# Kernel optimization log

Measured on AMD Instinct MI355X. Metric: run time of the kernel, lower is better.

The kernel has to match this reference:

```python
import jax, jax.numpy as jnp
import numpy as np

NEG_SLOPE = 0.01  # nn.LeakyReLU default

def leaky(x):
    return jnp.where(x >= 0, x, NEG_SLOPE * x)

def setup_inputs() -> dict:
    key = jax.random.key(0)
    ks = jax.random.split(key, 10)
    N, E, IN_DIM, OUT_DIM = 100000, 1600000, 128, 128
    indices = jax.random.randint(ks[0], (2, E), 0, N, dtype=jnp.int64 if jax.config.jax_enable_x64 else jnp.int32)
    features = jax.random.normal(ks[1], (N, IN_DIM), dtype=jnp.float32)
    s = 1.0 / np.sqrt(IN_DIM)
    W_att_w = jax.random.uniform(ks[2], (OUT_DIM, IN_DIM), minval=-s, maxval=s)
    W_att_b = jax.random.uniform(ks[3], (OUT_DIM,), minval=-s, maxval=s)
    W1_w = jax.random.uniform(ks[4], (OUT_DIM, IN_DIM), minval=-s, maxval=s)
    W1_b = jax.random.uniform(ks[5], (OUT_DIM,), minval=-s, maxval=s)
    W2_w = jax.random.uniform(ks[6], (OUT_DIM, OUT_DIM), minval=-s, maxval=s)
    W2_b = jax.random.uniform(ks[7], (OUT_DIM,), minval=-s, maxval=s)
    # xavier_uniform for a: gain*sqrt(6/(fan_in+fan_out)), fan_in=2*OUT_DIM, fan_out=1
    lim = float(np.sqrt(6.0 / (2 * OUT_DIM + 1)))
    a = jax.random.uniform(ks[8], (2 * OUT_DIM, 1), minval=-lim, maxval=lim)
    return {"indices": indices, "features": features, "num_nodes": N,
            "W_att_w": W_att_w, "W_att_b": W_att_b, "W1_w": W1_w, "W1_b": W1_b,
            "W2_w": W2_w, "W2_b": W2_b, "a": a}

def reference(indices, features, num_nodes, W_att_w, W_att_b, W1_w, W1_b, W2_w, W2_b, a):
    src, dst = indices[0], indices[1]
    out_dim = W_att_w.shape[0]
    # h_trans = W_att(features)
    h_trans = features @ W_att_w.T + W_att_b  # [N, D]
    # cat([src_h, dst_h]) @ a  ==  src_h @ a[:D] + dst_h @ a[D:]  (avoids materializing cat)
    a_src, a_dst = a[:out_dim], a[out_dim:]
    logits = leaky(h_trans[src] @ a_src + h_trans[dst] @ a_dst)  # [E, 1]
    # edge softmax over incoming edges of each dst (raw exp, as in original)
    exp_l = jnp.exp(logits)
    denom = jax.ops.segment_sum(exp_l, dst, num_segments=num_nodes)  # [N, 1]
    alpha = exp_l / (denom[dst] + 1e-9)  # [E, 1]
    # sparse.mm(adj_att, W1(features)) == segment_sum of alpha * msg[src] over dst
    h_msg = features @ W1_w.T + W1_b  # [N, D]
    h_neigh = jax.ops.segment_sum(alpha * h_msg[src], dst, num_segments=num_nodes)  # [N, D]
    h_self = features  # in_dim == out_dim branch
    term1 = h_self + h_neigh
    term2 = (h_self * h_neigh) @ W2_w.T + W2_b
    return leaky(term1 + term2)
```

## Files before the change

### kernel.cpp

```cpp
#include <hip/hip_runtime.h>

#define D 128
#define CAP 2560
typedef __attribute__((ext_vector_type(8))) short short8;
typedef __attribute__((ext_vector_type(4))) float f32x4;

__device__ __forceinline__ float leaky(float x){ return x >= 0.f ? x : 0.01f*x; }
__device__ __forceinline__ unsigned short f2bf(float x){
    unsigned u = __float_as_uint(x);
    u = (u + 0x7fffu + ((u>>16)&1u)) >> 16;
    return (unsigned short)u;
}
__device__ __forceinline__ short8 pack8m(f32x4 a, f32x4 b){
    short8 s;
    s[0]=(short)f2bf(a[0]); s[1]=(short)f2bf(a[1]);
    s[2]=(short)f2bf(a[2]); s[3]=(short)f2bf(a[3]);
    s[4]=(short)f2bf(b[0]); s[5]=(short)f2bf(b[1]);
    s[6]=(short)f2bf(b[2]); s[7]=(short)f2bf(b[3]);
    return s;
}

__global__ void k_prep(const float* __restrict__ Ww, const float* __restrict__ Wb,
                       const float* __restrict__ a, float* __restrict__ v,
                       const float* __restrict__ W1, const float* __restrict__ W2,
                       unsigned short* __restrict__ W1b, unsigned short* __restrict__ W2b){
    int b = blockIdx.x;
    if(b < 64){
        int i = b*256 + threadIdx.x;
        W1b[i] = f2bf(W1[i]);
        W2b[i] = f2bf(W2[i]);
        return;
    }
    int i = threadIdx.x; if(i >= 128) return;
    float vs=0.f, vd=0.f;
    for (int o=0;o<D;++o){ float w = Ww[o*D+i]; vs = fmaf(w, a[o], vs); vd = fmaf(w, a[D+o], vd); }
    v[i]=vs; v[D+i]=vd;
    if(i==0){
        float cs=0.f,cd=0.f;
        for(int o=0;o<D;++o){ cs=fmaf(Wb[o],a[o],cs); cd=fmaf(Wb[o],a[D+o],cd); }
        v[256]=cs; v[257]=cd;
    }
}

__global__ __launch_bounds__(256) void k_msgscal(const float* __restrict__ F,
        const unsigned short* __restrict__ W1b, const float* __restrict__ b1,
        const float* __restrict__ v, unsigned short* __restrict__ Hp,
        float* __restrict__ ss, float* __restrict__ sd, int N,
        const int* __restrict__ dst, unsigned* __restrict__ M,
        int E, int GT, int CHUNK, int NB){
    __shared__ __align__(16) unsigned short Wlds[17408];
    if((int)blockIdx.x >= GT){
        unsigned* h = (unsigned*)Wlds;
        for(int i=threadIdx.x;i<NB;i+=256) h[i]=0u;
        __syncthreads();
        int blk = (int)blockIdx.x - GT;
        int s = blk*CHUNK;
        int e = s+CHUNK < E ? s+CHUNK : E;
        for(int i=s+(int)threadIdx.x;i<e;i+=256) atomicAdd(&h[((unsigned)dst[i])>>6],1u);
        __syncthreads();
        for(int j=threadIdx.x;j<NB;j+=256) M[(size_t)j*256 + blk] = h[j];
        return;
    }
    #pragma unroll
    for(int k=0;k<8;++k){
        int idx = ((int)threadIdx.x + k*256)*8;
        int row = idx >> 7, col = idx & 127;
        *(short8*)(&Wlds[row*136 + col]) = *(const short8*)(W1b + idx);
    }
    __syncthreads();
    const int lane = threadIdx.x & 63, wv = threadIdx.x>>6;
    const int t = lane & 15, g = lane >> 4;
    float bb[8];
    #pragma unroll
    for(int j=0;j<8;++j) bb[j] = b1[j*16+t];
    const float c_s = v[256], c_d = v[257];
    const int Mt = (N+15)>>4;
    for(int rt = (int)blockIdx.x*4 + wv; rt < Mt; rt += GT*4){
        int row0 = rt*16 + t;
        int row = row0 < N ? row0 : N-1;
        const float* fr = F + (size_t)row*D + g*8;
        f32x4 acc[8];
        #pragma unroll
        for(int j=0;j<8;++j) acc[j] = (f32x4){0.f,0.f,0.f,0.f};
        float ds = 0.f, dd = 0.f;
        #pragma unroll
        for(int kk=0;kk<4;++kk){
            f32x4 lo = *(const f32x4*)(fr + kk*32);
            f32x4 hi = *(const f32x4*)(fr + kk*32 + 4);
            f32x4 vsl = *(const f32x4*)(v + kk*32 + g*8);
            f32x4 vsh = *(const f32x4*)(v + kk*32 + g*8 + 4);
            f32x4 vdl = *(const f32x4*)(v + D + kk*32 + g*8);
            f32x4 vdh = *(const f32x4*)(v + D + kk*32 + g*8 + 4);
            #pragma unroll
            for(int q=0;q<4;++q){
                ds = fmaf(lo[q], vsl[q], ds); ds = fmaf(hi[q], vsh[q], ds);
                dd = fmaf(lo[q], vdl[q], dd); dd = fmaf(hi[q], vdh[q], dd);
            }
            short8 af = pack8m(lo, hi);
            #pragma unroll
            for(int j=0;j<8;++j){
                short8 wfj = *(const short8*)(&Wlds[(j*16+t)*136 + kk*32 + g*8]);
                acc[j] = __builtin_amdgcn_mfma_f32_16x16x32_bf16(af, wfj, acc[j], 0,0,0);
            }
        }
        ds += __shfl_xor(ds,16); ds += __shfl_xor(ds,32);
        dd += __shfl_xor(dd,16); dd += __shfl_xor(dd,32);
        if(g==0 && row0 < N){ ss[row0] = ds + c_s; sd[row0] = dd + c_d; }
        #pragma unroll
        for(int r=0;r<4;++r){
            int rr = rt*16 + g*4 + r;
            if(rr < N){
                short8 h;
                #pragma unroll
                for(int j=0;j<8;++j) h[j] = (short)f2bf(acc[j][r] + bb[j]);
                *(short8*)(Hp + (size_t)rr*D + t*8) = h;
            }
        }
    }
}

__global__ __launch_bounds__(256) void k_scanA(const unsigned* __restrict__ M,
        unsigned* __restrict__ bsum, int n){
    __shared__ unsigned lds[4];
    int base = blockIdx.x*4096 + threadIdx.x*16;
    unsigned s=0;
    #pragma unroll
    for(int k=0;k<16;++k){ int i=base+k; if(i<n) s+=M[i]; }
    #pragma unroll
    for(int o=1;o<64;o<<=1) s += __shfl_xor(s,o);
    if((threadIdx.x&63)==0) lds[threadIdx.x>>6]=s;
    __syncthreads();
    if(threadIdx.x==0) bsum[blockIdx.x] = lds[0]+lds[1]+lds[2]+lds[3];
}

__global__ __launch_bounds__(256) void k_scanC(const unsigned* __restrict__ M,
        const unsigned* __restrict__ bsum, unsigned* __restrict__ Msc, int n, int nsb){
    __shared__ unsigned lds[4];
    __shared__ unsigned ps[2];
    int t = threadIdx.x;
    unsigned pv = (t < nsb && t < (int)blockIdx.x) ? bsum[t] : 0u;
    #pragma unroll
    for(int o=1;o<64;o<<=1) pv += __shfl_xor(pv,o);
    if((t&63)==0 && t<128) ps[t>>6]=pv;
    int base = blockIdx.x*4096 + t*16;
    unsigned v[16]; unsigned tsum=0;
    #pragma unroll
    for(int k=0;k<16;++k){ int i=base+k; v[k]=(i<n)?M[i]:0u; tsum+=v[k]; }
    unsigned x=tsum;
    #pragma unroll
    for(int o=1;o<64;o<<=1){ unsigned y=__shfl_up(x,(unsigned)o); if((t&63)>=o) x+=y; }
    if((t&63)==63) lds[t>>6]=x;
    __syncthreads();
    unsigned run = ps[0]+ps[1];
    for(int w=0;w<(t>>6);++w) run += lds[w];
    run += (x - tsum);
    #pragma unroll
    for(int k=0;k<16;++k){ int i=base+k; if(i<n) Msc[i]=run; run+=v[k]; }
}

__global__ __launch_bounds__(256) void k_bscatter(const int* __restrict__ src,
        const int* __restrict__ dst, const unsigned* __restrict__ Msc,
        const float* __restrict__ ss, const float* __restrict__ sdv,
        uint2* __restrict__ ew, int E, int NB, int CHUNK){
    __shared__ unsigned hoff[1600];
    int blk = blockIdx.x, NBLKg = gridDim.x;
    for(int i=threadIdx.x;i<NB;i+=256) hoff[i] = Msc[(size_t)i*NBLKg + blk];
    __syncthreads();
    int s0 = blk*CHUNK;
    int e1 = s0+CHUNK < E ? s0+CHUNK : E;
    for(int i=s0+(int)threadIdx.x;i<e1;i+=256){
        int d = dst[i];
        int s = src[i];
        float w = __expf(leaky(ss[s] + sdv[d]));
        unsigned p = atomicAdd(&hoff[((unsigned)d)>>6], 1u);
        ew[p] = make_uint2(((unsigned)s<<6)|((unsigned)d&63u), __float_as_uint(w));
    }
}

__device__ __forceinline__ void fma8(float* acc, uint4 u, float w){
    acc[0]=fmaf(w,__uint_as_float(u.x<<16),acc[0]);
    acc[1]=fmaf(w,__uint_as_float(u.x&0xffff0000u),acc[1]);
    acc[2]=fmaf(w,__uint_as_float(u.y<<16),acc[2]);
    acc[3]=fmaf(w,__uint_as_float(u.y&0xffff0000u),acc[3]);
    acc[4]=fmaf(w,__uint_as_float(u.z<<16),acc[4]);
    acc[5]=fmaf(w,__uint_as_float(u.z&0xffff0000u),acc[5]);
    acc[6]=fmaf(w,__uint_as_float(u.w<<16),acc[6]);
    acc[7]=fmaf(w,__uint_as_float(u.w&0xffff0000u),acc[7]);
}

__global__ __launch_bounds__(256) void k_gfine(const uint2* __restrict__ ew,
        const unsigned* __restrict__ Msc, const unsigned short* __restrict__ Hp,
        float* __restrict__ out, int N, int NB, int E){
    __shared__ uint2 sed[CAP+16];
    __shared__ unsigned cA[64], cB[64], loff[64];
    __shared__ unsigned begS, endS;
    const int b = blockIdx.x;
    const int dbase = b<<6;
    const int tid = threadIdx.x;
    if(tid==0){
        begS = Msc[(size_t)b*256];
        endS = (b+1 < NB) ? Msc[(size_t)(b+1)*256] : (unsigned)E;
    }
    if(tid<64){ cA[tid]=0u; cB[tid]=0u; }
    __syncthreads();
    const unsigned beg = begS;
    const unsigned size = endS - begS;
    const int wv = tid>>6, l = tid&63;
    const int g = l>>4, t = l&15;
    const unsigned toff = (unsigned)t*16u;

    if(size <= CAP){
        for(unsigned i=tid; i<size; i+=256)
            atomicAdd(&cA[ew[beg+i].x & 63u], 1u);
        __syncthreads();
        if(tid<64){
            unsigned c = cA[tid];
            unsigned x = c;
            #pragma unroll
            for(int o=1;o<64;o<<=1){ unsigned y = __shfl_up(x,(unsigned)o); if(tid>=o) x += y; }
            loff[tid] = x - c;
        }
        __syncthreads();
        for(unsigned i=tid; i<size; i+=256){
            uint2 p = ew[beg+i];
            unsigned dl = p.x & 63u;
            unsigned r = atomicAdd(&cB[dl], 1u);
            sed[loff[dl]+r] = make_uint2(p.x>>6, p.y);
        }
        for(unsigned i=size+tid; i<size+16u; i+=256) sed[i] = make_uint2(0u,0u);
        __syncthreads();
        #pragma unroll 1
        for(int i=0;i<16;++i){
            int dl = i*4 + wv;
            int d = dbase + dl;
            if(d >= N) continue;
            unsigned kb = loff[dl], ke = kb + cB[dl];
            float acc[8];
            #pragma unroll
            for(int j=0;j<8;++j) acc[j]=0.f;
            float den = 0.f;
            unsigned e = kb + g;
            uint2 p0 = sed[e];
            uint4 u0 = *(const uint4*)((const char*)Hp + ((p0.x<<8) + toff));
            uint2 p1 = sed[e+4];
            uint4 u1 = *(const uint4*)((const char*)Hp + ((p1.x<<8) + toff));
            while(e < ke){
                float w0 = __uint_as_float(p0.y);
                fma8(acc, u0, w0);
                p0 = sed[e+8];
                u0 = *(const uint4*)((const char*)Hp + ((p0.x<<8) + toff));
                float w1 = (e+4 < ke) ? __uint_as_float(p1.y) : 0.f;
                fma8(acc, u1, w1);
                p1 = sed[e+12];
                u1 = *(const uint4*)((const char*)Hp + ((p1.x<<8) + toff));
                den += w0 + w1;
                e += 8;
            }
            #pragma unroll
            for(int j=0;j<8;++j){
                acc[j] += __shfl_xor(acc[j],16);
                acc[j] += __shfl_xor(acc[j],32);
            }
            den += __shfl_xor(den,16);
            den += __shfl_xor(den,32);
            float inv = 1.f/(den + 1e-9f);
            int c = g*32 + t;
            out[(size_t)d*D + c]      = acc[g*2]  * inv;
            out[(size_t)d*D + c + 16] = acc[g*2+1]* inv;
        }
    } else {
        #pragma unroll 1
        for(int i=0;i<16;++i){
            int dl = i*4 + wv;
            int d = dbase + dl;
            if(d >= N) continue;
            float acc[8];
            #pragma unroll
            for(int j=0;j<8;++j) acc[j]=0.f;
            float den = 0.f;
            for(unsigned e2 = beg + (unsigned)g; e2 < beg + size; e2 += 4){
                uint2 p = ew[e2];
                if((int)(p.x & 63u) != dl) continue;
                float w = __uint_as_float(p.y);
                uint4 u = *(const uint4*)((const char*)Hp + (((p.x>>6)<<8) + toff));
                fma8(acc, u, w);
                den += w;
            }
            #pragma unroll
            for(int j=0;j<8;++j){
                acc[j] += __shfl_xor(acc[j],16);
                acc[j] += __shfl_xor(acc[j],32);
            }
            den += __shfl_xor(den,16);
            den += __shfl_xor(den,32);
            float inv = 1.f/(den + 1e-9f);
            int c = g*32 + t;
            out[(size_t)d*D + c]      = acc[g*2]  * inv;
            out[(size_t)d*D + c + 16] = acc[g*2+1]* inv;
        }
    }
}

__global__ __launch_bounds__(256) void k_final(const float* __restrict__ F,
        const unsigned short* __restrict__ W2b, const float* __restrict__ b2,
        float* __restrict__ out, int N, int GF){
    __shared__ __align__(16) unsigned short Wlds[17408];
    #pragma unroll
    for(int k=0;k<8;++k){
        int idx = ((int)threadIdx.x + k*256)*8;
        int row = idx >> 7, col = idx & 127;
        *(short8*)(&Wlds[row*136 + col]) = *(const short8*)(W2b + idx);
    }
    __syncthreads();
    const int lane = threadIdx.x & 63, wv = threadIdx.x>>6;
    const int t = lane & 15, g = lane >> 4;
    float bb[8];
    #pragma unroll
    for(int j=0;j<8;++j) bb[j] = b2[j*16+t];
    const int Mt = (N+15)>>4;
    for(int rt = (int)blockIdx.x*4 + wv; rt < Mt; rt += GF*4){
        int row = rt*16 + t; if(row>=N) row = N-1;
        const float* fr = F   + (size_t)row*D + g*8;
        const float* hr = out + (size_t)row*D + g*8;
        f32x4 acc[8];
        #pragma unroll
        for(int j=0;j<8;++j) acc[j] = (f32x4){0.f,0.f,0.f,0.f};
        #pragma unroll
        for(int kk=0;kk<4;++kk){
            f32x4 flo = *(const f32x4*)(fr + kk*32);
            f32x4 fhi = *(const f32x4*)(fr + kk*32 + 4);
            f32x4 hlo = *(const f32x4*)(hr + kk*32);
            f32x4 hhi = *(const f32x4*)(hr + kk*32 + 4);
            short8 af = pack8m(flo*hlo, fhi*hhi);
            #pragma unroll
            for(int j=0;j<8;++j){
                short8 wfj = *(const short8*)(&Wlds[(j*16+t)*136 + kk*32 + g*8]);
                acc[j] = __builtin_amdgcn_mfma_f32_16x16x32_bf16(af, wfj, acc[j], 0,0,0);
            }
        }
        #pragma unroll
        for(int r=0;r<4;++r){
            int rr = rt*16 + g*4 + r;
            if(rr < N){
                #pragma unroll
                for(int j=0;j<8;++j){
                    int c = j*16 + t;
                    float f = F[(size_t)rr*D + c];
                    float h = out[(size_t)rr*D + c];
                    out[(size_t)rr*D + c] = leaky(f + h + acc[j][r] + bb[j]);
                }
            }
        }
    }
}

extern "C" void kernel_launch(void* const* d_in, const int* in_sizes, int n_in,
                              void* d_out, int out_size, void* d_ws, size_t ws_size,
                              hipStream_t stream) {
    const int*   idx  = (const int*)  d_in[0];
    const float* F    = (const float*)d_in[1];
    const float* Waw  = (const float*)d_in[3];
    const float* Wab  = (const float*)d_in[4];
    const float* W1w  = (const float*)d_in[5];
    const float* W1b  = (const float*)d_in[6];
    const float* W2w  = (const float*)d_in[7];
    const float* W2b  = (const float*)d_in[8];
    const float* a    = (const float*)d_in[9];
    float* out = (float*)d_out;

    const int E = in_sizes[0]/2;
    const int N = in_sizes[1]/D;
    const int* srcp = idx;
    const int* dstp = idx + E;

    const int NBLK = 256;
    const int CHUNK = (E + NBLK - 1)/NBLK;
    const int NB = (N + 63)/64;
    const int NT = NB*NBLK;
    const int NSB = (NT + 4095)/4096;

    uint2*    ew   = (uint2*)d_ws;
    unsigned short* Hp  = (unsigned short*)(ew + E);
    unsigned short* W1c = Hp + (size_t)N*D;
    unsigned short* W2c = W1c + 16384;
    float*    ss   = (float*)(W2c + 16384);
    float*    sd   = ss + N;
    float*    v    = sd + N;
    unsigned* M    = (unsigned*)(v + 320);
    unsigned* Msc  = M + NT;
    unsigned* bsum = Msc + NT + 2;

    const int Mt = (N+15)/16;
    const int GT = (Mt+3)/4;
    const int GF = GT;

    k_prep    <<<65, 256, 0, stream>>>(Waw, Wab, a, v, W1w, W2w, W1c, W2c);
    k_msgscal <<<GT+NBLK, 256, 0, stream>>>(F, W1c, W1b, v, Hp, ss, sd, N,
                                            dstp, M, E, GT, CHUNK, NB);
    k_scanA   <<<NSB, 256, 0, stream>>>(M, bsum, NT);
    k_scanC   <<<NSB, 256, 0, stream>>>(M, bsum, Msc, NT, NSB);
    k_bscatter<<<NBLK, 256, 0, stream>>>(srcp, dstp, Msc, ss, sd, ew, E, NB, CHUNK);
    k_gfine   <<<NB, 256, 0, stream>>>(ew, Msc, Hp, out, N, NB, E);
    k_final   <<<GF, 256, 0, stream>>>(F, W2c, W2b, out, N, GF);
}
```

Measured before the change: 185.7 us.

## Fuse block-sum scan pass into histogram kernel and cap GEMM grid size

Each histogram block now computes its per-superblock partial sums from LDS and atomically adds them into bsum, which k_prep zeroes. This removes the separate k_scanA launch. The histogram LDS clear is widened to a fixed 1600 entries so the 16-entry groups past NB read as zero. The message-GEMM and final grids change from a size derived from N to a fixed 512 blocks using grid-stride loops, which adds global atomics and the risk of fewer blocks than the work would otherwise get.

```diff
diff --git a/kernel.cpp b/kernel.cpp
--- a/kernel.cpp
+++ b/kernel.cpp
@@ -23,12 +23,17 @@
 __global__ void k_prep(const float* __restrict__ Ww, const float* __restrict__ Wb,
                        const float* __restrict__ a, float* __restrict__ v,
                        const float* __restrict__ W1, const float* __restrict__ W2,
-                       unsigned short* __restrict__ W1b, unsigned short* __restrict__ W2b){
+                       unsigned short* __restrict__ W1b, unsigned short* __restrict__ W2b,
+                       unsigned* __restrict__ bsum, int NSB){
     int b = blockIdx.x;
     if(b < 64){
         int i = b*256 + threadIdx.x;
         W1b[i] = f2bf(W1[i]);
         W2b[i] = f2bf(W2[i]);
+        return;
+    }
+    if(b == 65){
+        if((int)threadIdx.x < NSB) bsum[threadIdx.x] = 0u;
         return;
     }
     int i = threadIdx.x; if(i >= 128) return;
@@ -47,11 +52,11 @@
         const float* __restrict__ v, unsigned short* __restrict__ Hp,
         float* __restrict__ ss, float* __restrict__ sd, int N,
         const int* __restrict__ dst, unsigned* __restrict__ M,
-        int E, int GT, int CHUNK, int NB){
+        unsigned* __restrict__ bsum, int E, int GT, int CHUNK, int NB, int NSB){
     __shared__ __align__(16) unsigned short Wlds[17408];
     if((int)blockIdx.x >= GT){
         unsigned* h = (unsigned*)Wlds;
-        for(int i=threadIdx.x;i<NB;i+=256) h[i]=0u;
+        for(int i=threadIdx.x;i<1600;i+=256) h[i]=0u;
         __syncthreads();
         int blk = (int)blockIdx.x - GT;
         int s = blk*CHUNK;
@@ -59,6 +64,11 @@
         for(int i=s+(int)threadIdx.x;i<e;i+=256) atomicAdd(&h[((unsigned)dst[i])>>6],1u);
         __syncthreads();
         for(int j=threadIdx.x;j<NB;j+=256) M[(size_t)j*256 + blk] = h[j];
+        for(int sb=threadIdx.x; sb<NSB; sb+=256){
+            unsigned sum=0;
+            for(int k=0;k<16;++k) sum += h[sb*16+k];
+            atomicAdd(&bsum[sb], sum);
+        }
         return;
     }
     #pragma unroll
@@ -117,20 +127,6 @@
             }
         }
     }
-}
-
-__global__ __launch_bounds__(256) void k_scanA(const unsigned* __restrict__ M,
-        unsigned* __restrict__ bsum, int n){
-    __shared__ unsigned lds[4];
-    int base = blockIdx.x*4096 + threadIdx.x*16;
-    unsigned s=0;
-    #pragma unroll
-    for(int k=0;k<16;++k){ int i=base+k; if(i<n) s+=M[i]; }
-    #pragma unroll
-    for(int o=1;o<64;o<<=1) s += __shfl_xor(s,o);
-    if((threadIdx.x&63)==0) lds[threadIdx.x>>6]=s;
-    __syncthreads();
-    if(threadIdx.x==0) bsum[blockIdx.x] = lds[0]+lds[1]+lds[2]+lds[3];
 }
 
 __global__ __launch_bounds__(256) void k_scanC(const unsigned* __restrict__ M,
@@ -390,14 +386,12 @@
     unsigned* Msc  = M + NT;
     unsigned* bsum = Msc + NT + 2;
 
-    const int Mt = (N+15)/16;
-    const int GT = (Mt+3)/4;
-    const int GF = GT;
-
-    k_prep    <<<65, 256, 0, stream>>>(Waw, Wab, a, v, W1w, W2w, W1c, W2c);
+    const int GT = 512;
+    const int GF = 512;
+
+    k_prep    <<<66, 256, 0, stream>>>(Waw, Wab, a, v, W1w, W2w, W1c, W2c, bsum, NSB);
     k_msgscal <<<GT+NBLK, 256, 0, stream>>>(F, W1c, W1b, v, Hp, ss, sd, N,
-                                            dstp, M, E, GT, CHUNK, NB);
-    k_scanA   <<<NSB, 256, 0, stream>>>(M, bsum, NT);
+                                            dstp, M, bsum, E, GT, CHUNK, NB, NSB);
     k_scanC   <<<NSB, 256, 0, stream>>>(M, bsum, Msc, NT, NSB);
     k_bscatter<<<NBLK, 256, 0, stream>>>(srcp, dstp, Msc, ss, sd, ew, E, NB, CHUNK);
     k_gfine   <<<NB, 256, 0, stream>>>(ew, Msc, Hp, out, N, NB, E);
```

After: 181.8 us. -2.1%, faster.
